# Kernel tuning notes

Measured on AMD Instinct MI355X. Metric: run time of the kernel, lower is better.

The kernel has to match this reference:

```python
import jax, jax.numpy as jnp
import numpy as np

B, IN, OUT, FAN = 2048, 4096, 4096, 64

def setup_inputs() -> dict:
    key = jax.random.key(0)
    k1, k2, k3, k4 = jax.random.split(key, 4)
    input = jax.random.normal(k1, (B, IN), dtype=jnp.float32)
    condensed_weight = jax.random.normal(k2, (OUT, FAN), dtype=jnp.float32) * 0.05
    bias = jax.random.normal(k3, (OUT,), dtype=jnp.float32) * 0.05
    input_mask = jax.random.randint(k4, (OUT, FAN), 0, IN, dtype=jnp.int64)
    return {"input": input, "condensed_weight": condensed_weight,
            "bias": bias, "input_mask": input_mask}

def reference(input, condensed_weight, bias, input_mask):
    # Per output neuron o: sum_f input[b, idx[o,f]] * w[o,f] + bias[o]
    # gathered: [B, OUT, FAN] -- the structured-sparse gather
    gathered = jnp.take(input, input_mask, axis=1)
    return jnp.einsum("bof,of->bo", gathered, condensed_weight) + bias
```

## Files before the change

kernel.cpp:

```cpp
#include <hip/hip_runtime.h>

#define B_DIM   2048
#define IN_DIM  4096
#define OUT_DIM 4096
#define FAN     64


typedef float v2f __attribute__((ext_vector_type(2)));

__device__ __forceinline__ unsigned bf16_rne(float f) {
    unsigned u = __float_as_uint(f);
    return (u + 0x7fffu + ((u >> 16) & 1u)) >> 16;
}

__global__ __launch_bounds__(256) void pack_kernel(
    const float* __restrict__ input, uint4* __restrict__ wsp)
{
    const int idx = blockIdx.x * 256 + threadIdx.x;
    const int t   = idx >> 11;
    const int c0  = (idx & 2047) << 1;

    const float* p = input + (size_t)t * 8 * IN_DIM + c0;
    const float2 r0 = *reinterpret_cast<const float2*>(p + 0 * IN_DIM);
    const float2 r1 = *reinterpret_cast<const float2*>(p + 1 * IN_DIM);
    const float2 r2 = *reinterpret_cast<const float2*>(p + 2 * IN_DIM);
    const float2 r3 = *reinterpret_cast<const float2*>(p + 3 * IN_DIM);
    const float2 r4 = *reinterpret_cast<const float2*>(p + 4 * IN_DIM);
    const float2 r5 = *reinterpret_cast<const float2*>(p + 5 * IN_DIM);
    const float2 r6 = *reinterpret_cast<const float2*>(p + 6 * IN_DIM);
    const float2 r7 = *reinterpret_cast<const float2*>(p + 7 * IN_DIM);

    uint4 a, b;
    a.x = bf16_rne(r0.x) | (bf16_rne(r1.x) << 16);
    a.y = bf16_rne(r2.x) | (bf16_rne(r3.x) << 16);
    a.z = bf16_rne(r4.x) | (bf16_rne(r5.x) << 16);
    a.w = bf16_rne(r6.x) | (bf16_rne(r7.x) << 16);
    b.x = bf16_rne(r0.y) | (bf16_rne(r1.y) << 16);
    b.y = bf16_rne(r2.y) | (bf16_rne(r3.y) << 16);
    b.z = bf16_rne(r4.y) | (bf16_rne(r5.y) << 16);
    b.w = bf16_rne(r6.y) | (bf16_rne(r7.y) << 16);

    uint4* q = wsp + (size_t)t * IN_DIM + c0;
    q[0] = a;
    q[1] = b;
}

__global__ __launch_bounds__(512, 2) void condensed_kernel(
    const uint4* __restrict__ wsp,
    const float* __restrict__ weight,
    const float* __restrict__ bias,
    const int*   __restrict__ mask,
    float*       __restrict__ out)
{
    __shared__ __align__(16) uint4 lds[IN_DIM];

    const int tid   = threadIdx.x;
    const int o     = blockIdx.y * 512 + tid;
    const int bseg  = blockIdx.x * 32;
    const int tbase = bseg >> 3;

    unsigned paddr[FAN / 2];
    float    wv[FAN];
    {
        const int4*   mv = reinterpret_cast<const int4*>(mask)     + o * (FAN / 4);
        const float4* wp = reinterpret_cast<const float4*>(weight) + o * (FAN / 4);
        #pragma unroll
        for (int j = 0; j < FAN / 4; ++j) {
            int4   m4 = mv[j];
            float4 w4 = wp[j];
            paddr[2*j+0] = ((unsigned)m4.x << 4) | ((unsigned)m4.y << 20);
            paddr[2*j+1] = ((unsigned)m4.z << 4) | ((unsigned)m4.w << 20);
            wv[4*j+0] = w4.x;
            wv[4*j+1] = w4.y;
            wv[4*j+2] = w4.z;
            wv[4*j+3] = w4.w;
        }
    }
    const float bv = bias[o];
    const char* ldsb = reinterpret_cast<const char*>(lds);

    #pragma unroll
    for (int bt = 0; bt < 4; ++bt) {
        __syncthreads();

        const uint4* src = wsp + (size_t)(tbase + bt) * IN_DIM + tid;
        #pragma unroll
        for (int it = 0; it < 8; ++it) {
            __builtin_amdgcn_global_load_lds(
                (const __attribute__((address_space(1))) unsigned*)(src + it * 512),
                (__attribute__((address_space(3))) unsigned*)(lds + it * 512 + tid),
                16, 0, 0);
        }

        __syncthreads();

        v2f a01 = {0.f, 0.f}, a23 = {0.f, 0.f}, a45 = {0.f, 0.f}, a67 = {0.f, 0.f};
        #pragma unroll
        for (int jj = 0; jj < FAN / 2; ++jj) {
            const unsigned pa = paddr[jj];
            const uint4 g0 = *reinterpret_cast<const uint4*>(ldsb + (pa & 0xffffu));
            const uint4 g1 = *reinterpret_cast<const uint4*>(ldsb + (pa >> 16));
            {
                const v2f w2 = {wv[2*jj+0], wv[2*jj+0]};
                v2f v;
                v.x = __uint_as_float(g0.x << 16);
                v.y = __uint_as_float(g0.x & 0xffff0000u);
                a01 = __builtin_elementwise_fma(v, w2, a01);
                v.x = __uint_as_float(g0.y << 16);
                v.y = __uint_as_float(g0.y & 0xffff0000u);
                a23 = __builtin_elementwise_fma(v, w2, a23);
                v.x = __uint_as_float(g0.z << 16);
                v.y = __uint_as_float(g0.z & 0xffff0000u);
                a45 = __builtin_elementwise_fma(v, w2, a45);
                v.x = __uint_as_float(g0.w << 16);
                v.y = __uint_as_float(g0.w & 0xffff0000u);
                a67 = __builtin_elementwise_fma(v, w2, a67);
            }
            {
                const v2f w2 = {wv[2*jj+1], wv[2*jj+1]};
                v2f v;
                v.x = __uint_as_float(g1.x << 16);
                v.y = __uint_as_float(g1.x & 0xffff0000u);
                a01 = __builtin_elementwise_fma(v, w2, a01);
                v.x = __uint_as_float(g1.y << 16);
                v.y = __uint_as_float(g1.y & 0xffff0000u);
                a23 = __builtin_elementwise_fma(v, w2, a23);
                v.x = __uint_as_float(g1.z << 16);
                v.y = __uint_as_float(g1.z & 0xffff0000u);
                a45 = __builtin_elementwise_fma(v, w2, a45);
                v.x = __uint_as_float(g1.w << 16);
                v.y = __uint_as_float(g1.w & 0xffff0000u);
                a67 = __builtin_elementwise_fma(v, w2, a67);
            }
        }

        float* op = out + (size_t)(bseg + bt * 8) * OUT_DIM + o;
        op[0 * OUT_DIM] = a01.x + bv;
        op[1 * OUT_DIM] = a01.y + bv;
        op[2 * OUT_DIM] = a23.x + bv;
        op[3 * OUT_DIM] = a23.y + bv;
        op[4 * OUT_DIM] = a45.x + bv;
        op[5 * OUT_DIM] = a45.y + bv;
        op[6 * OUT_DIM] = a67.x + bv;
        op[7 * OUT_DIM] = a67.y + bv;
    }
}

extern "C" void kernel_launch(void* const* d_in, const int* in_sizes, int n_in,
                              void* d_out, int out_size, void* d_ws, size_t ws_size,
                              hipStream_t stream) {
    const float* input  = (const float*)d_in[0];
    const float* weight = (const float*)d_in[1];
    const float* bias   = (const float*)d_in[2];
    const int*   mask   = (const int*)d_in[3];
    float*       out    = (float*)d_out;
    uint4*       wsp    = (uint4*)d_ws;

    pack_kernel<<<2048, 256, 0, stream>>>(input, wsp);
    dim3 grid(64, 8);
    condensed_kernel<<<grid, 512, 0, stream>>>(wsp, weight, bias, mask, out);
}
```

Baseline: 140.0 us.

## Double-buffer LDS tiles to overlap global-to-LDS DMA with gather compute

```diff
diff --git a/kernel.cpp b/kernel.cpp
--- a/kernel.cpp
+++ b/kernel.cpp
@@ -45,18 +45,86 @@
     q[1] = b;
 }
 
-__global__ __launch_bounds__(512, 2) void condensed_kernel(
+template <unsigned BASE>
+__device__ __forceinline__ void gather_tile(
+    const char* ldsb, const unsigned* paddr, const float* wv,
+    float bv, float* op)
+{
+    v2f a01 = {0.f, 0.f}, a23 = {0.f, 0.f}, a45 = {0.f, 0.f}, a67 = {0.f, 0.f};
+    #pragma unroll
+    for (int jj = 0; jj < FAN / 2; ++jj) {
+        const unsigned pa = paddr[jj];
+        const uint4 g0 = *reinterpret_cast<const uint4*>(ldsb + BASE + (pa & 0xffffu));
+        const uint4 g1 = *reinterpret_cast<const uint4*>(ldsb + BASE + (pa >> 16));
+        {
+            const v2f w2 = {wv[2*jj+0], wv[2*jj+0]};
+            v2f v;
+            v.x = __uint_as_float(g0.x << 16);
+            v.y = __uint_as_float(g0.x & 0xffff0000u);
+            a01 = __builtin_elementwise_fma(v, w2, a01);
+            v.x = __uint_as_float(g0.y << 16);
+            v.y = __uint_as_float(g0.y & 0xffff0000u);
+            a23 = __builtin_elementwise_fma(v, w2, a23);
+            v.x = __uint_as_float(g0.z << 16);
+            v.y = __uint_as_float(g0.z & 0xffff0000u);
+            a45 = __builtin_elementwise_fma(v, w2, a45);
+            v.x = __uint_as_float(g0.w << 16);
+            v.y = __uint_as_float(g0.w & 0xffff0000u);
+            a67 = __builtin_elementwise_fma(v, w2, a67);
+        }
+        {
+            const v2f w2 = {wv[2*jj+1], wv[2*jj+1]};
+            v2f v;
+            v.x = __uint_as_float(g1.x << 16);
+            v.y = __uint_as_float(g1.x & 0xffff0000u);
+            a01 = __builtin_elementwise_fma(v, w2, a01);
+            v.x = __uint_as_float(g1.y << 16);
+            v.y = __uint_as_float(g1.y & 0xffff0000u);
+            a23 = __builtin_elementwise_fma(v, w2, a23);
+            v.x = __uint_as_float(g1.z << 16);
+            v.y = __uint_as_float(g1.z & 0xffff0000u);
+            a45 = __builtin_elementwise_fma(v, w2, a45);
+            v.x = __uint_as_float(g1.w << 16);
+            v.y = __uint_as_float(g1.w & 0xffff0000u);
+            a67 = __builtin_elementwise_fma(v, w2, a67);
+        }
+    }
+    op[0 * OUT_DIM] = a01.x + bv;
+    op[1 * OUT_DIM] = a01.y + bv;
+    op[2 * OUT_DIM] = a23.x + bv;
+    op[3 * OUT_DIM] = a23.y + bv;
+    op[4 * OUT_DIM] = a45.x + bv;
+    op[5 * OUT_DIM] = a45.y + bv;
+    op[6 * OUT_DIM] = a67.x + bv;
+    op[7 * OUT_DIM] = a67.y + bv;
+}
+
+__device__ __forceinline__ void dma_tile(const uint4* __restrict__ wsp,
+                                         uint4* lds, int tile, int tid, int buf)
+{
+    const uint4* src = wsp + (size_t)tile * IN_DIM + tid;
+    uint4*       dst = lds + buf * IN_DIM + tid;
+    #pragma unroll
+    for (int it = 0; it < 8; ++it) {
+        __builtin_amdgcn_global_load_lds(
+            (const __attribute__((address_space(1))) unsigned*)(src + it * 512),
+            (__attribute__((address_space(3))) unsigned*)(dst + it * 512),
+            16, 0, 0);
+    }
+}
+
+__global__ __launch_bounds__(512, 1) void condensed_kernel(
     const uint4* __restrict__ wsp,
     const float* __restrict__ weight,
     const float* __restrict__ bias,
     const int*   __restrict__ mask,
     float*       __restrict__ out)
 {
-    __shared__ __align__(16) uint4 lds[IN_DIM];
+    extern __shared__ __align__(16) uint4 lds[];
 
     const int tid   = threadIdx.x;
     const int o     = blockIdx.y * 512 + tid;
-    const int bseg  = blockIdx.x * 32;
+    const int bseg  = blockIdx.x * 64;
     const int tbase = bseg >> 3;
 
     unsigned paddr[FAN / 2];
@@ -79,70 +147,23 @@
     const float bv = bias[o];
     const char* ldsb = reinterpret_cast<const char*>(lds);
 
-    #pragma unroll
-    for (int bt = 0; bt < 4; ++bt) {
+    dma_tile(wsp, lds, tbase, tid, 0);
+    __syncthreads();
+
+    for (int hp = 0; hp < 4; ++hp) {
+        const int t0 = hp * 2;
+
+        dma_tile(wsp, lds, tbase + t0 + 1, tid, 1);
+        gather_tile<0u>(ldsb, paddr, wv, bv,
+                        out + (size_t)(bseg + 8 * t0) * OUT_DIM + o);
         __syncthreads();
 
-        const uint4* src = wsp + (size_t)(tbase + bt) * IN_DIM + tid;
-        #pragma unroll
-        for (int it = 0; it < 8; ++it) {
-            __builtin_amdgcn_global_load_lds(
-                (const __attribute__((address_space(1))) unsigned*)(src + it * 512),
-                (__attribute__((address_space(3))) unsigned*)(lds + it * 512 + tid),
-                16, 0, 0);
+        if (hp < 3) {
+            dma_tile(wsp, lds, tbase + t0 + 2, tid, 0);
         }
-
+        gather_tile<65536u>(ldsb, paddr, wv, bv,
+                            out + (size_t)(bseg + 8 * t0 + 8) * OUT_DIM + o);
         __syncthreads();
-
-        v2f a01 = {0.f, 0.f}, a23 = {0.f, 0.f}, a45 = {0.f, 0.f}, a67 = {0.f, 0.f};
-        #pragma unroll
-        for (int jj = 0; jj < FAN / 2; ++jj) {
-            const unsigned pa = paddr[jj];
-            const uint4 g0 = *reinterpret_cast<const uint4*>(ldsb + (pa & 0xffffu));
-            const uint4 g1 = *reinterpret_cast<const uint4*>(ldsb + (pa >> 16));
-            {
-                const v2f w2 = {wv[2*jj+0], wv[2*jj+0]};
-                v2f v;
-                v.x = __uint_as_float(g0.x << 16);
-                v.y = __uint_as_float(g0.x & 0xffff0000u);
-                a01 = __builtin_elementwise_fma(v, w2, a01);
-                v.x = __uint_as_float(g0.y << 16);
-                v.y = __uint_as_float(g0.y & 0xffff0000u);
-                a23 = __builtin_elementwise_fma(v, w2, a23);
-                v.x = __uint_as_float(g0.z << 16);
-                v.y = __uint_as_float(g0.z & 0xffff0000u);
-                a45 = __builtin_elementwise_fma(v, w2, a45);
-                v.x = __uint_as_float(g0.w << 16);
-                v.y = __uint_as_float(g0.w & 0xffff0000u);
-                a67 = __builtin_elementwise_fma(v, w2, a67);
-            }
-            {
-                const v2f w2 = {wv[2*jj+1], wv[2*jj+1]};
-                v2f v;
-                v.x = __uint_as_float(g1.x << 16);
-                v.y = __uint_as_float(g1.x & 0xffff0000u);
-                a01 = __builtin_elementwise_fma(v, w2, a01);
-                v.x = __uint_as_float(g1.y << 16);
-                v.y = __uint_as_float(g1.y & 0xffff0000u);
-                a23 = __builtin_elementwise_fma(v, w2, a23);
-                v.x = __uint_as_float(g1.z << 16);
-                v.y = __uint_as_float(g1.z & 0xffff0000u);
-                a45 = __builtin_elementwise_fma(v, w2, a45);
-                v.x = __uint_as_float(g1.w << 16);
-                v.y = __uint_as_float(g1.w & 0xffff0000u);
-                a67 = __builtin_elementwise_fma(v, w2, a67);
-            }
-        }
-
-        float* op = out + (size_t)(bseg + bt * 8) * OUT_DIM + o;
-        op[0 * OUT_DIM] = a01.x + bv;
-        op[1 * OUT_DIM] = a01.y + bv;
-        op[2 * OUT_DIM] = a23.x + bv;
-        op[3 * OUT_DIM] = a23.y + bv;
-        op[4 * OUT_DIM] = a45.x + bv;
-        op[5 * OUT_DIM] = a45.y + bv;
-        op[6 * OUT_DIM] = a67.x + bv;
-        op[7 * OUT_DIM] = a67.y + bv;
     }
 }
 
@@ -157,6 +178,9 @@
     uint4*       wsp    = (uint4*)d_ws;
 
     pack_kernel<<<2048, 256, 0, stream>>>(input, wsp);
-    dim3 grid(64, 8);
-    condensed_kernel<<<grid, 512, 0, stream>>>(wsp, weight, bias, mask, out);
+
+    hipFuncSetAttribute(reinterpret_cast<const void*>(condensed_kernel),
+                        hipFuncAttributeMaxDynamicSharedMemorySize, 131072);
+    dim3 grid(32, 8);
+    condensed_kernel<<<grid, 512, 131072, stream>>>(wsp, weight, bias, mask, out);
 }
```

Measured after the change: 133.1 us. -5.0%, faster.
